# Kernel optimization log

Hardware: AMD Instinct MI355X
Metric: run time of the kernel (lower is better)

## Reference

```python
import jax, jax.numpy as jnp
import numpy as np

IN_FEATURES = 128
HIDDEN_DIM = 128
ALPHA = 0.2
NEG_INF = -9e15


def setup_inputs() -> dict:
    key = jax.random.key(0)
    k1, k2, k3, k4, k5 = jax.random.split(key, 5)
    N, n_context = 20000, 32
    h_i = jax.random.normal(k1, (N, IN_FEATURES), dtype=jnp.float32)
    context_indices = jax.random.randint(k2, (N, n_context), 0, N, dtype=jnp.int64)
    # learned params (torch nn.Linear default init scale ~ U(-1/sqrt(fan_in), 1/sqrt(fan_in)))
    s1 = 1.0 / np.sqrt(IN_FEATURES)
    s2 = 1.0 / np.sqrt(2 * HIDDEN_DIM)
    W_i = jax.random.uniform(k3, (IN_FEATURES, HIDDEN_DIM), jnp.float32, -s1, s1)
    W_j = jax.random.uniform(k4, (IN_FEATURES, HIDDEN_DIM), jnp.float32, -s1, s1)
    ka, kb = jax.random.split(k5)
    a_w = jax.random.uniform(ka, (2 * HIDDEN_DIM, 1), jnp.float32, -s2, s2)
    a_b = jax.random.uniform(kb, (1,), jnp.float32, -s2, s2)
    return {"h_i": h_i, "context_indices": context_indices,
            "W_i": W_i, "W_j": W_j, "a_w": a_w, "a_b": a_b}


def reference(h_i, context_indices, W_i, W_j, a_w, a_b):
    N, n_context = context_indices.shape
    # -1 padding maps to an extra zero row (torch indexes -1 -> last row of padded table)
    h_padded = jnp.concatenate([h_i, jnp.zeros((1, h_i.shape[1]), h_i.dtype)], axis=0)
    idx = jnp.where(context_indices >= 0, context_indices, N)
    h_j = h_padded[idx]                      # [N, n_context, in_features]
    Wh_i = h_i @ W_i                         # [N, hidden]
    Wh_j = jnp.einsum('ncf,fh->nch', h_j, W_j)  # [N, n_context, hidden]
    # attention_layer(cat(Wh_i, Wh_j)) split into two matvecs (same math as concat)
    a_i, a_j = a_w[:HIDDEN_DIM, 0], a_w[HIDDEN_DIM:, 0]
    e = Wh_i @ a_i                           # [N]
    e = e[:, None] + Wh_j @ a_j + a_b[0]     # [N, n_context]
    e = jax.nn.leaky_relu(e, ALPHA)
    e = jnp.where(context_indices >= 0, e, NEG_INF)
    attn = jax.nn.softmax(e, axis=1)         # [N, n_context]
    h_prime = jnp.einsum('nc,nch->nh', attn, Wh_j)
    return h_prime
```

## Files before the change

kernel.cpp:

```cpp
#include <hip/hip_runtime.h>
#include <hip/hip_fp16.h>

#define GAT_ALPHA 0.2f
#define GAT_NEG_INF -9.0e15f

typedef _Float16 half8_t __attribute__((ext_vector_type(8)));
typedef _Float16 half4_t __attribute__((ext_vector_type(4)));
typedef float f32x4 __attribute__((ext_vector_type(4)));

__global__ void gat_precompute_vi(const float* __restrict__ Wi,
                                  const float* __restrict__ aw,
                                  float* __restrict__ vi) {
    int f = threadIdx.x;
    float s = 0.f;
    #pragma unroll 8
    for (int h = 0; h < 128; ++h)
        s = fmaf(Wi[f * 128 + h], aw[h], s);
    vi[f] = s;
}

__global__ __launch_bounds__(256) void gat_transform_mfma(
    const float* __restrict__ h, const float* __restrict__ Wj,
    const float* __restrict__ aw, const float* __restrict__ ab,
    const float* __restrict__ vi,
    __half* __restrict__ Wh16, float* __restrict__ e1, float* __restrict__ e2,
    int N) {
    __shared__ _Float16 sWt[128 * 136];
    const int t = threadIdx.x;
    for (int i = t; i < 128 * 128; i += 256) {
        int k = i >> 7, n = i & 127;
        sWt[n * 136 + k] = (_Float16)Wj[i];
    }
    __syncthreads();

    const int wave = t >> 6, lane = t & 63, q = lane >> 4, l16 = lane & 15;
    const float abv = ab[0];

    float vir[4][8];
    {
        const float4* vi4 = (const float4*)vi;
        #pragma unroll
        for (int s = 0; s < 4; ++s) {
            float4 u0 = vi4[s * 8 + q * 2];
            float4 u1 = vi4[s * 8 + q * 2 + 1];
            vir[s][0] = u0.x; vir[s][1] = u0.y; vir[s][2] = u0.z; vir[s][3] = u0.w;
            vir[s][4] = u1.x; vir[s][5] = u1.y; vir[s][6] = u1.z; vir[s][7] = u1.w;
        }
    }
    float ajr[8];
    #pragma unroll
    for (int c = 0; c < 8; ++c) ajr[c] = aw[128 + c * 16 + l16];

    const int ntiles = (N + 15) >> 4;
    for (int tile = blockIdx.x * 4 + wave; tile < ntiles; tile += gridDim.x * 4) {
        const int base = tile << 4;
        int row = base + l16; if (row >= N) row = N - 1;
        const float* hp = h + (size_t)row * 128 + q * 8;

        half8_t af[4];
        float pe1 = 0.f;
        #pragma unroll
        for (int s = 0; s < 4; ++s) {
            float4 f0 = *(const float4*)(hp + s * 32);
            float4 f1 = *(const float4*)(hp + s * 32 + 4);
            pe1 = fmaf(f0.x, vir[s][0], pe1); pe1 = fmaf(f0.y, vir[s][1], pe1);
            pe1 = fmaf(f0.z, vir[s][2], pe1); pe1 = fmaf(f0.w, vir[s][3], pe1);
            pe1 = fmaf(f1.x, vir[s][4], pe1); pe1 = fmaf(f1.y, vir[s][5], pe1);
            pe1 = fmaf(f1.z, vir[s][6], pe1); pe1 = fmaf(f1.w, vir[s][7], pe1);
            half8_t a;
            a[0] = (_Float16)f0.x; a[1] = (_Float16)f0.y;
            a[2] = (_Float16)f0.z; a[3] = (_Float16)f0.w;
            a[4] = (_Float16)f1.x; a[5] = (_Float16)f1.y;
            a[6] = (_Float16)f1.z; a[7] = (_Float16)f1.w;
            af[s] = a;
        }

        f32x4 acc[8];
        #pragma unroll
        for (int c = 0; c < 8; ++c) { f32x4 z = {0.f, 0.f, 0.f, 0.f}; acc[c] = z; }

        const _Float16* wbase = sWt + l16 * 136 + q * 8;
        #pragma unroll
        for (int s = 0; s < 4; ++s) {
            #pragma unroll
            for (int c = 0; c < 8; ++c) {
                half8_t bf = *(const half8_t*)(wbase + c * (16 * 136) + s * 32);
                acc[c] = __builtin_amdgcn_mfma_f32_16x16x32_f16(af[s], bf, acc[c], 0, 0, 0);
            }
        }

        const bool full = (base + 16 <= N);
        float pe2[4] = {0.f, 0.f, 0.f, 0.f};
        #pragma unroll
        for (int c = 0; c < 8; ++c) {
            #pragma unroll
            for (int r = 0; r < 4; ++r) {
                float v = acc[c][r];
                pe2[r] = fmaf(v, ajr[c], pe2[r]);
                int rr = base + q * 4 + r;
                if (full || rr < N)
                    Wh16[(size_t)rr * 128 + (c * 16 + l16)] = __float2half(v);
            }
        }
        #pragma unroll
        for (int r = 0; r < 4; ++r) {
            pe2[r] += __shfl_xor(pe2[r], 1);
            pe2[r] += __shfl_xor(pe2[r], 2);
            pe2[r] += __shfl_xor(pe2[r], 4);
            pe2[r] += __shfl_xor(pe2[r], 8);
        }
        if (l16 == 0) {
            #pragma unroll
            for (int r = 0; r < 4; ++r) {
                int rr = base + q * 4 + r;
                if (rr < N) e2[rr] = pe2[r];
            }
        }
        pe1 += __shfl_xor(pe1, 16);
        pe1 += __shfl_xor(pe1, 32);
        if (lane < 16) {
            int rr = base + lane;
            if (rr < N) e1[rr] = pe1 + abv;
        }
    }
}

__global__ __launch_bounds__(256) void gat_gather2(
    const int* __restrict__ ctx, const float* __restrict__ e1,
    const float* __restrict__ e2, const __half* __restrict__ Wh16,
    float* __restrict__ out, int N) {
    const int t = threadIdx.x;
    const int wave = t >> 6, lane = t & 63, hf = lane >> 5, l = lane & 31;
    const int pair = blockIdx.x * 4 + wave;
    if (pair * 2 >= N) return;
    const int n = pair * 2 + hf;
    const bool okn = (n < N);
    const int nn = okn ? n : (N - 1);

    const int iv = ctx[(size_t)nn * 32 + l];
    const bool valid = (iv >= 0);
    const int j = valid ? iv : 0;
    float lg = e1[nn] + e2[j];
    lg = fmaxf(lg, GAT_ALPHA * lg);
    lg = valid ? lg : GAT_NEG_INF;
    float m = lg;
    #pragma unroll
    for (int s = 16; s; s >>= 1) m = fmaxf(m, __shfl_xor(m, s));
    float p = valid ? __expf(lg - m) : 0.f;
    float ss = p;
    #pragma unroll
    for (int s = 16; s; s >>= 1) ss += __shfl_xor(ss, s);
    p = (ss > 0.f) ? p / ss : 0.f;

    const int offB = j << 8;
    float a0 = 0.f, a1 = 0.f, a2 = 0.f, a3 = 0.f;
    const char* wb = (const char*)Wh16 + (size_t)(l * 8);
    #pragma unroll 8
    for (int cc = 0; cc < 32; ++cc) {
        int off = __shfl(offB, cc, 32);
        float w = __shfl(p, cc, 32);
        half4_t hv = *(const half4_t*)(wb + off);
        a0 = fmaf(w, (float)hv[0], a0);
        a1 = fmaf(w, (float)hv[1], a1);
        a2 = fmaf(w, (float)hv[2], a2);
        a3 = fmaf(w, (float)hv[3], a3);
    }
    if (okn) {
        float4 o; o.x = a0; o.y = a1; o.z = a2; o.w = a3;
        ((float4*)(out + (size_t)n * 128))[l] = o;
    }
}

extern "C" void kernel_launch(void* const* d_in, const int* in_sizes, int n_in,
                              void* d_out, int out_size, void* d_ws, size_t ws_size,
                              hipStream_t stream) {
    const float* h   = (const float*)d_in[0];
    const int*   ctx = (const int*)d_in[1];
    const float* Wi  = (const float*)d_in[2];
    const float* Wj  = (const float*)d_in[3];
    const float* aw  = (const float*)d_in[4];
    const float* ab  = (const float*)d_in[5];
    float* out = (float*)d_out;
    const int N = in_sizes[0] / 128;

    float* vi = (float*)d_ws;
    float* e1 = vi + 256;
    float* e2 = e1 + N;
    __half* Wh16 = (__half*)(e2 + N);

    const int ntiles = (N + 15) >> 4;
    int g1 = (ntiles + 3) / 4; if (g1 > 160) g1 = 160;
    const int pairs = (N + 1) / 2;

    gat_precompute_vi<<<1, 128, 0, stream>>>(Wi, aw, vi);
    gat_transform_mfma<<<g1, 256, 0, stream>>>(h, Wj, aw, ab, vi, Wh16, e1, e2, N);
    gat_gather2<<<(pairs + 3) / 4, 256, 0, stream>>>(ctx, e1, e2, Wh16, out, N);
}
```

Before: 102.3 us.

## Fold vi precompute into transform kernel and gather four nodes per wave

Each transform block now computes the Wi·a_i vector into shared memory, which removes the separate single-block precompute launch and its global round trip. The grid cap of 160 on the transform kernel is dropped, so one 16-row tile goes to each wave. The gather kernel handles four nodes per wave with 16 lanes each, loading 8 halves (16 bytes) per lane and two context indices per lane, which doubles load width and halves the shuffle reductions. In exchange every block redundantly recomputes vi, and the wider per-lane work raises register use.

Measured after the change: 101.5 us. About the same (-0.7%).

```diff
diff --git a/kernel.cpp b/kernel.cpp
--- a/kernel.cpp
+++ b/kernel.cpp
@@ -5,28 +5,30 @@
 #define GAT_NEG_INF -9.0e15f
 
 typedef _Float16 half8_t __attribute__((ext_vector_type(8)));
-typedef _Float16 half4_t __attribute__((ext_vector_type(4)));
 typedef float f32x4 __attribute__((ext_vector_type(4)));
 
-__global__ void gat_precompute_vi(const float* __restrict__ Wi,
-                                  const float* __restrict__ aw,
-                                  float* __restrict__ vi) {
-    int f = threadIdx.x;
-    float s = 0.f;
-    #pragma unroll 8
-    for (int h = 0; h < 128; ++h)
-        s = fmaf(Wi[f * 128 + h], aw[h], s);
-    vi[f] = s;
-}
-
 __global__ __launch_bounds__(256) void gat_transform_mfma(
-    const float* __restrict__ h, const float* __restrict__ Wj,
-    const float* __restrict__ aw, const float* __restrict__ ab,
-    const float* __restrict__ vi,
+    const float* __restrict__ h, const float* __restrict__ Wi,
+    const float* __restrict__ Wj, const float* __restrict__ aw,
+    const float* __restrict__ ab,
     __half* __restrict__ Wh16, float* __restrict__ e1, float* __restrict__ e2,
     int N) {
     __shared__ _Float16 sWt[128 * 136];
+    __shared__ float svi[128];
     const int t = threadIdx.x;
+
+    if (t < 128) {
+        const float4* wrow = (const float4*)(Wi + (size_t)t * 128);
+        const float4* a4 = (const float4*)aw;
+        float s = 0.f;
+        #pragma unroll
+        for (int i = 0; i < 32; ++i) {
+            float4 w = wrow[i], a = a4[i];
+            s = fmaf(w.x, a.x, s); s = fmaf(w.y, a.y, s);
+            s = fmaf(w.z, a.z, s); s = fmaf(w.w, a.w, s);
+        }
+        svi[t] = s;
+    }
     for (int i = t; i < 128 * 128; i += 256) {
         int k = i >> 7, n = i & 127;
         sWt[n * 136 + k] = (_Float16)Wj[i];
@@ -37,15 +39,12 @@
     const float abv = ab[0];
 
     float vir[4][8];
-    {
-        const float4* vi4 = (const float4*)vi;
-        #pragma unroll
-        for (int s = 0; s < 4; ++s) {
-            float4 u0 = vi4[s * 8 + q * 2];
-            float4 u1 = vi4[s * 8 + q * 2 + 1];
-            vir[s][0] = u0.x; vir[s][1] = u0.y; vir[s][2] = u0.z; vir[s][3] = u0.w;
-            vir[s][4] = u1.x; vir[s][5] = u1.y; vir[s][6] = u1.z; vir[s][7] = u1.w;
-        }
+    #pragma unroll
+    for (int s = 0; s < 4; ++s) {
+        float4 u0 = *(const float4*)(svi + s * 32 + q * 8);
+        float4 u1 = *(const float4*)(svi + s * 32 + q * 8 + 4);
+        vir[s][0] = u0.x; vir[s][1] = u0.y; vir[s][2] = u0.z; vir[s][3] = u0.w;
+        vir[s][4] = u1.x; vir[s][5] = u1.y; vir[s][6] = u1.z; vir[s][7] = u1.w;
     }
     float ajr[8];
     #pragma unroll
@@ -125,49 +124,59 @@
     }
 }
 
-__global__ __launch_bounds__(256) void gat_gather2(
+__global__ __launch_bounds__(256) void gat_gather4(
     const int* __restrict__ ctx, const float* __restrict__ e1,
     const float* __restrict__ e2, const __half* __restrict__ Wh16,
     float* __restrict__ out, int N) {
     const int t = threadIdx.x;
-    const int wave = t >> 6, lane = t & 63, hf = lane >> 5, l = lane & 31;
-    const int pair = blockIdx.x * 4 + wave;
-    if (pair * 2 >= N) return;
-    const int n = pair * 2 + hf;
+    const int wave = t >> 6, lane = t & 63, qid = lane >> 4, l = lane & 15;
+    const int widx = blockIdx.x * 4 + wave;
+    if (widx * 4 >= N) return;
+    const int n = widx * 4 + qid;
     const bool okn = (n < N);
     const int nn = okn ? n : (N - 1);
 
-    const int iv = ctx[(size_t)nn * 32 + l];
-    const bool valid = (iv >= 0);
-    const int j = valid ? iv : 0;
-    float lg = e1[nn] + e2[j];
-    lg = fmaxf(lg, GAT_ALPHA * lg);
-    lg = valid ? lg : GAT_NEG_INF;
-    float m = lg;
-    #pragma unroll
-    for (int s = 16; s; s >>= 1) m = fmaxf(m, __shfl_xor(m, s));
-    float p = valid ? __expf(lg - m) : 0.f;
-    float ss = p;
-    #pragma unroll
-    for (int s = 16; s; s >>= 1) ss += __shfl_xor(ss, s);
-    p = (ss > 0.f) ? p / ss : 0.f;
-
-    const int offB = j << 8;
+    int2 ij = ((const int2*)(ctx + (size_t)nn * 32))[l];
+    const bool v0 = (ij.x >= 0), v1 = (ij.y >= 0);
+    const int j0 = v0 ? ij.x : 0, j1 = v1 ? ij.y : 0;
+    const float eb = e1[nn];
+    float lg0 = eb + e2[j0], lg1 = eb + e2[j1];
+    lg0 = fmaxf(lg0, GAT_ALPHA * lg0);
+    lg1 = fmaxf(lg1, GAT_ALPHA * lg1);
+    lg0 = v0 ? lg0 : GAT_NEG_INF;
+    lg1 = v1 ? lg1 : GAT_NEG_INF;
+    float m = fmaxf(lg0, lg1);
+    #pragma unroll
+    for (int s = 8; s; s >>= 1) m = fmaxf(m, __shfl_xor(m, s, 16));
+    float p0 = v0 ? __expf(lg0 - m) : 0.f;
+    float p1 = v1 ? __expf(lg1 - m) : 0.f;
+    float ss = p0 + p1;
+    #pragma unroll
+    for (int s = 8; s; s >>= 1) ss += __shfl_xor(ss, s, 16);
+    const float inv = (ss > 0.f) ? __frcp_rn(ss) : 0.f;
+    p0 *= inv; p1 *= inv;
+
+    const int o0 = j0 << 8, o1 = j1 << 8;
     float a0 = 0.f, a1 = 0.f, a2 = 0.f, a3 = 0.f;
-    const char* wb = (const char*)Wh16 + (size_t)(l * 8);
+    float a4 = 0.f, a5 = 0.f, a6 = 0.f, a7 = 0.f;
+    const char* wb = (const char*)Wh16 + (size_t)(l * 16);
     #pragma unroll 8
     for (int cc = 0; cc < 32; ++cc) {
-        int off = __shfl(offB, cc, 32);
-        float w = __shfl(p, cc, 32);
-        half4_t hv = *(const half4_t*)(wb + off);
-        a0 = fmaf(w, (float)hv[0], a0);
-        a1 = fmaf(w, (float)hv[1], a1);
-        a2 = fmaf(w, (float)hv[2], a2);
-        a3 = fmaf(w, (float)hv[3], a3);
+        const int src = cc >> 1;
+        float w   = __shfl((cc & 1) ? p1 : p0, src, 16);
+        int   off = __shfl((cc & 1) ? o1 : o0, src, 16);
+        half8_t hv = *(const half8_t*)(wb + off);
+        a0 = fmaf(w, (float)hv[0], a0); a1 = fmaf(w, (float)hv[1], a1);
+        a2 = fmaf(w, (float)hv[2], a2); a3 = fmaf(w, (float)hv[3], a3);
+        a4 = fmaf(w, (float)hv[4], a4); a5 = fmaf(w, (float)hv[5], a5);
+        a6 = fmaf(w, (float)hv[6], a6); a7 = fmaf(w, (float)hv[7], a7);
     }
     if (okn) {
-        float4 o; o.x = a0; o.y = a1; o.z = a2; o.w = a3;
-        ((float4*)(out + (size_t)n * 128))[l] = o;
+        float4* orow = (float4*)(out + (size_t)n * 128);
+        float4 u; u.x = a0; u.y = a1; u.z = a2; u.w = a3;
+        float4 v; v.x = a4; v.y = a5; v.z = a6; v.w = a7;
+        orow[2 * l] = u;
+        orow[2 * l + 1] = v;
     }
 }
 
@@ -183,16 +192,15 @@
     float* out = (float*)d_out;
     const int N = in_sizes[0] / 128;
 
-    float* vi = (float*)d_ws;
-    float* e1 = vi + 256;
+    float* e1 = (float*)d_ws;
     float* e2 = e1 + N;
     __half* Wh16 = (__half*)(e2 + N);
 
     const int ntiles = (N + 15) >> 4;
-    int g1 = (ntiles + 3) / 4; if (g1 > 160) g1 = 160;
-    const int pairs = (N + 1) / 2;
-
-    gat_precompute_vi<<<1, 128, 0, stream>>>(Wi, aw, vi);
-    gat_transform_mfma<<<g1, 256, 0, stream>>>(h, Wj, aw, ab, vi, Wh16, e1, e2, N);
-    gat_gather2<<<(pairs + 3) / 4, 256, 0, stream>>>(ctx, e1, e2, Wh16, out, N);
+    const int g1 = (ntiles + 3) / 4;
+    const int nquad = (N + 3) / 4;
+    const int g2 = (nquad + 3) / 4;
+
+    gat_transform_mfma<<<g1, 256, 0, stream>>>(h, Wi, Wj, aw, ab, Wh16, e1, e2, N);
+    gat_gather4<<<g2, 256, 0, stream>>>(ctx, e1, e2, Wh16, out, N);
 }
```
